# Kernel optimization log

Measured on AMD Instinct MI355X. Metric: run time of the kernel, lower is better.

Reference implementation:

```python
import jax, jax.numpy as jnp
import numpy as np

N_IN = 250000
N_OUT = 500000
INC = 256
OUTC = 128
KVOL = 8  # 2x2x2 transposed-conv kernel volume
BN_EPS = 1e-5


def setup_inputs() -> dict:
    key = jax.random.key(0)
    k1, k2, k3 = jax.random.split(key, 3)
    x = jax.random.normal(k1, (N_IN, INC), dtype=jnp.float32)
    # sparse conv weight: one [inc, outc] matrix per kernel offset
    W = jax.random.normal(k2, (KVOL, INC, OUTC), dtype=jnp.float32) * 0.02
    gamma = jnp.ones((OUTC,), dtype=jnp.float32)
    beta = jnp.zeros((OUTC,), dtype=jnp.float32)
    # kernel map: destination output voxel for each (kernel offset, input voxel)
    out_idx = jax.random.randint(k3, (KVOL, N_IN), 0, N_OUT, dtype=jnp.int32)
    return {"x": x, "W": W, "gamma": gamma, "beta": beta,
            "out_idx": out_idx, "n_out": N_OUT}


def reference(x, W, gamma, beta, out_idx, n_out):
    # --- sparse transposed conv3d: gather-matmul-scatter per kernel offset ---
    out = jnp.zeros((n_out, W.shape[-1]), dtype=x.dtype)
    for k in range(W.shape[0]):  # fixed small kernel volume (8)
        out = out.at[out_idx[k]].add(x @ W[k])
    # --- BatchNorm (training-mode batch stats over all output voxels) ---
    mean = jnp.mean(out, axis=0)
    var = jnp.mean(jnp.square(out - mean), axis=0)
    y = (out - mean) * jax.lax.rsqrt(var + BN_EPS) * gamma + beta
    return y
```

## Files before the change

### kernel.cpp

```cpp
#include <hip/hip_runtime.h>
#include <hip/hip_bf16.h>
#include <stdint.h>

#define N_IN 250000
#define N_OUT 500000
#define INC 256
#define OUTC 128
#define KVOL 8
#define NTOT (KVOL * N_IN)
#define BN_EPS 1e-5f

typedef __bf16 bf16x8_t __attribute__((ext_vector_type(8)));
typedef __bf16 bf16x4_t __attribute__((ext_vector_type(4)));
typedef float f32x4_t __attribute__((ext_vector_type(4)));
typedef uint32_t u32x4_t __attribute__((ext_vector_type(4)));

__device__ __forceinline__ __bf16 f2bf(float x) {
  union { float f; uint32_t u; } v; v.f = x;
  uint32_t r = v.u + 0x7FFFu + ((v.u >> 16) & 1u);
  union { uint16_t s; __bf16 b; } o; o.s = (uint16_t)(r >> 16);
  return o.b;
}

__device__ __forceinline__ uint32_t pack2bf(float lo, float hi) {
  union { float f; uint32_t u; } a, b; a.f = lo; b.f = hi;
  uint32_t ra = a.u + 0x7FFFu + ((a.u >> 16) & 1u);
  uint32_t rb = b.u + 0x7FFFu + ((b.u >> 16) & 1u);
  return (ra >> 16) | (rb & 0xFFFF0000u);
}

__device__ __forceinline__ float bflo(uint32_t w) {
  union { uint32_t u; float f; } v; v.u = w << 16; return v.f;
}
__device__ __forceinline__ float bfhi(uint32_t w) {
  union { uint32_t u; float f; } v; v.u = w & 0xFFFF0000u; return v.f;
}

__global__ void wconv_kernel(const float* __restrict__ W, __bf16* __restrict__ Wt) {
  int f = blockIdx.x * blockDim.x + threadIdx.x;
  if (f >= KVOL * OUTC * INC) return;
  int i = f & (INC - 1);
  int o = (f >> 8) & (OUTC - 1);
  int k = f >> 15;
  Wt[f] = f2bf(W[(k * INC + i) * OUTC + o]);
}


__global__ void hist_kernel(const int* __restrict__ oidx, int* __restrict__ cnt) {
  int g = blockIdx.x * 256 + threadIdx.x;
  if (g < NTOT) atomicAdd(&cnt[oidx[g]], 1);
}

__global__ void scan1_kernel(const int* __restrict__ cnt, int* __restrict__ offs,
                             int* __restrict__ bsum) {
  __shared__ int sd[256];
  int t = threadIdx.x;
  int base = blockIdx.x * 1024 + t * 4;
  int v0 = 0, v1 = 0, v2 = 0, v3 = 0;
  if (base + 3 < N_OUT) {
    int4 v = *(const int4*)&cnt[base];
    v0 = v.x; v1 = v.y; v2 = v.z; v3 = v.w;
  } else {
    if (base     < N_OUT) v0 = cnt[base];
    if (base + 1 < N_OUT) v1 = cnt[base + 1];
    if (base + 2 < N_OUT) v2 = cnt[base + 2];
  }
  int s = v0 + v1 + v2 + v3;
  sd[t] = s; __syncthreads();
  for (int o = 1; o < 256; o <<= 1) {
    int a = (t >= o) ? sd[t - o] : 0;
    __syncthreads();
    sd[t] += a;
    __syncthreads();
  }
  int excl = sd[t] - s;
  if (base     < N_OUT) offs[base]     = excl;
  if (base + 1 < N_OUT) offs[base + 1] = excl + v0;
  if (base + 2 < N_OUT) offs[base + 2] = excl + v0 + v1;
  if (base + 3 < N_OUT) offs[base + 3] = excl + v0 + v1 + v2;
  if (t == 255) bsum[blockIdx.x] = sd[255];
}

__global__ void scan2_kernel(const int* __restrict__ bsum, int* __restrict__ bsumx, int nb) {
  __shared__ int sd[512];
  int t = threadIdx.x;
  int s = (t < nb) ? bsum[t] : 0;
  sd[t] = s; __syncthreads();
  for (int o = 1; o < 512; o <<= 1) {
    int a = (t >= o) ? sd[t - o] : 0;
    __syncthreads();
    sd[t] += a;
    __syncthreads();
  }
  if (t < nb) bsumx[t] = sd[t] - s;
}

__global__ void scan3_kernel(int* __restrict__ offs, int* __restrict__ cursor,
                             const int* __restrict__ bsumx) {
  int g = blockIdx.x * 256 + threadIdx.x;
  if (g < N_OUT) {
    int v = offs[g] + bsumx[g >> 10];
    offs[g] = v;
    cursor[g] = v;
  }
  if (g == 0) offs[N_OUT] = NTOT;
}

__global__ void fill_kernel(const int* __restrict__ oidx, int* __restrict__ cursor,
                            int* __restrict__ slot) {
  int g = blockIdx.x * 256 + threadIdx.x;
  if (g < NTOT) {
    int d = oidx[g];
    slot[g] = atomicAdd(&cursor[d], 1);
  }
}


#define TM 64
#define LDS_STRIDE 264

__global__ __launch_bounds__(512, 1) void gemm_store_kernel(
    const float* __restrict__ x, const __bf16* __restrict__ Wt,
    const int* __restrict__ slot, char* __restrict__ partials) {
  __shared__ __bf16 xs[TM * LDS_STRIDE];
  __shared__ __align__(16) uint2 stg[8][16][34];
  const int t = threadIdx.x;
  const int row0 = blockIdx.x * TM;

  #pragma unroll
  for (int i = 0; i < 8; ++i) {
    int f = t + i * 512;
    int r = f >> 6;
    int c4 = f & 63;
    int grow = row0 + r;
    f32x4_t v = {0.f, 0.f, 0.f, 0.f};
    if (grow < N_IN)
      v = __builtin_nontemporal_load((const f32x4_t*)x + (size_t)grow * 64 + c4);
    bf16x4_t bv;
    bv[0] = f2bf(v[0]); bv[1] = f2bf(v[1]); bv[2] = f2bf(v[2]); bv[3] = f2bf(v[3]);
    *(bf16x4_t*)&xs[r * LDS_STRIDE + c4 * 4] = bv;
  }
  __syncthreads();

  const int w  = t >> 6;
  const int l  = t & 63;
  const int lr = l & 15;
  const int lg = l >> 4;

  f32x4_t accT[8][4];
  #pragma unroll
  for (int n = 0; n < 8; ++n)
    #pragma unroll
    for (int m = 0; m < 4; ++m)
      accT[n][m] = (f32x4_t){0.f, 0.f, 0.f, 0.f};

  const __bf16* Wk = Wt + (size_t)w * OUTC * INC;

  #pragma unroll
  for (int s = 0; s < 8; ++s) {
    bf16x8_t a[4], b[8];
    #pragma unroll
    for (int m = 0; m < 4; ++m)
      a[m] = *(const bf16x8_t*)&xs[(m * 16 + lr) * LDS_STRIDE + s * 32 + lg * 8];
    #pragma unroll
    for (int n = 0; n < 8; ++n)
      b[n] = *(const bf16x8_t*)&Wk[(n * 16 + lr) * INC + s * 32 + lg * 8];
    #pragma unroll
    for (int n = 0; n < 8; ++n)
      #pragma unroll
      for (int m = 0; m < 4; ++m)
        accT[n][m] = __builtin_amdgcn_mfma_f32_16x16x32_bf16(b[n], a[m], accT[n][m], 0, 0, 0);
  }

  const int r2 = l >> 2;
  const int p  = l & 3;
  const int sbase = w * N_IN + row0;
  #pragma unroll
  for (int m = 0; m < 4; ++m) {
    #pragma unroll
    for (int n = 0; n < 8; ++n) {
      uint2 pk;
      pk.x = pack2bf(accT[n][m][0], accT[n][m][1]);
      pk.y = pack2bf(accT[n][m][2], accT[n][m][3]);
      stg[w][lr][n * 4 + lg] = pk;
    }
    asm volatile("s_waitcnt lgkmcnt(0)" ::: "memory");
    __builtin_amdgcn_wave_barrier();
    int grow = row0 + m * 16 + r2;
    if (grow < N_IN) {
      int gs = slot[sbase + m * 16 + r2];
      const u32x4_t* rp = (const u32x4_t*)&stg[w][r2][0];
      char* dst = partials + (size_t)gs * 256 + p * 64;
      #pragma unroll
      for (int q = 0; q < 4; ++q)
        *(u32x4_t*)(dst + q * 16) = rp[p * 4 + q];
    }
    __builtin_amdgcn_wave_barrier();
  }
}


__global__ __launch_bounds__(256) void reduce_stats_kernel(
    const char* __restrict__ partials, const int* __restrict__ offs,
    char* __restrict__ accb, float* __restrict__ stats) {
  const int t = threadIdx.x;
  const int lane16 = t & 15;
  const int grp = t >> 4;
  float s[8], q[8];
  #pragma unroll
  for (int i = 0; i < 8; ++i) { s[i] = 0.f; q[i] = 0.f; }

  for (int d = blockIdx.x * 16 + grp; d < N_OUT; d += gridDim.x * 16) {
    int j0 = offs[d], j1 = offs[d + 1];
    float a[8];
    #pragma unroll
    for (int i = 0; i < 8; ++i) a[i] = 0.f;
    for (int j = j0; j < j1; ++j) {
      u32x4_t v = __builtin_nontemporal_load(
          (const u32x4_t*)(partials + (size_t)j * 256 + lane16 * 16));
      a[0] += bflo(v[0]); a[1] += bfhi(v[0]);
      a[2] += bflo(v[1]); a[3] += bfhi(v[1]);
      a[4] += bflo(v[2]); a[5] += bfhi(v[2]);
      a[6] += bflo(v[3]); a[7] += bfhi(v[3]);
    }
    u32x4_t o;
    o[0] = pack2bf(a[0], a[1]); o[1] = pack2bf(a[2], a[3]);
    o[2] = pack2bf(a[4], a[5]); o[3] = pack2bf(a[6], a[7]);
    *(u32x4_t*)(accb + (size_t)d * 512 + lane16 * 16) = o;
    #pragma unroll
    for (int u = 0; u < 4; ++u) {
      float f0 = bflo(o[u]), f1 = bfhi(o[u]);
      s[2 * u] += f0;     q[2 * u] += f0 * f0;
      s[2 * u + 1] += f1; q[2 * u + 1] += f1 * f1;
    }
  }

  __shared__ float reds[16][16][8];
  __shared__ float redq[16][16][8];
  #pragma unroll
  for (int i = 0; i < 8; ++i) { reds[grp][lane16][i] = s[i]; redq[grp][lane16][i] = q[i]; }
  __syncthreads();
  if (t < 128) {
    float acc = 0.f;
    #pragma unroll
    for (int g2 = 0; g2 < 16; ++g2) acc += reds[g2][t >> 3][t & 7];
    atomicAdd(&stats[t], acc);
  } else {
    int c = t - 128;
    float acc = 0.f;
    #pragma unroll
    for (int g2 = 0; g2 < 16; ++g2) acc += redq[g2][c >> 3][c & 7];
    atomicAdd(&stats[128 + c], acc);
  }
}

__global__ void norm_kernel(char* __restrict__ outb, const float* __restrict__ stats,
                            const float* __restrict__ gamma, const float* __restrict__ beta) {
  const int t = threadIdx.x;
  const int j = t & 15;
  const int ro = t >> 4;
  const float inv_n = 1.0f / (float)N_OUT;
  float sc[8], sh[8];
  #pragma unroll
  for (int i = 0; i < 8; ++i) {
    int c = j * 8 + i;
    float mean = stats[c] * inv_n;
    float var  = stats[128 + c] * inv_n - mean * mean;
    float s = gamma[c] * rsqrtf(var + BN_EPS);
    sc[i] = s;
    sh[i] = beta[c] - mean * s;
  }
  for (int r = blockIdx.x * 16 + ro; r < N_OUT; r += gridDim.x * 16) {
    u32x4_t v = *(const u32x4_t*)(outb + (size_t)r * 512 + j * 16);
    f32x4_t o0, o1;
    #pragma unroll
    for (int u = 0; u < 4; ++u) {
      float f0 = bflo(v[u]) * sc[2 * u] + sh[2 * u];
      float f1 = bfhi(v[u]) * sc[2 * u + 1] + sh[2 * u + 1];
      if (u < 2) { o0[2 * u] = f0; o0[2 * u + 1] = f1; }
      else       { o1[2 * (u - 2)] = f0; o1[2 * (u - 2) + 1] = f1; }
    }
    __builtin_nontemporal_store(o0, (f32x4_t*)(outb + (size_t)r * 512 + j * 32));
    __builtin_nontemporal_store(o1, (f32x4_t*)(outb + (size_t)r * 512 + j * 32 + 16));
  }
}


__global__ __launch_bounds__(512, 1) void gemm_scatter_f32_kernel(
    const float* __restrict__ x, const __bf16* __restrict__ Wt,
    const int* __restrict__ out_idx, float* __restrict__ acc) {
  __shared__ __bf16 xs[TM * LDS_STRIDE];
  const int t = threadIdx.x;
  const int row0 = blockIdx.x * TM;
  #pragma unroll
  for (int i = 0; i < 8; ++i) {
    int f = t + i * 512;
    int r = f >> 6;
    int c4 = f & 63;
    int grow = row0 + r;
    float4 v = make_float4(0.f, 0.f, 0.f, 0.f);
    if (grow < N_IN) v = ((const float4*)x)[(size_t)grow * 64 + c4];
    bf16x4_t bv;
    bv[0] = f2bf(v.x); bv[1] = f2bf(v.y); bv[2] = f2bf(v.z); bv[3] = f2bf(v.w);
    *(bf16x4_t*)&xs[r * LDS_STRIDE + c4 * 4] = bv;
  }
  __syncthreads();
  const int w = t >> 6, l = t & 63, lr = l & 15, lg = l >> 4;
  f32x4_t accr[4][8];
  #pragma unroll
  for (int m = 0; m < 4; ++m)
    #pragma unroll
    for (int n = 0; n < 8; ++n)
      accr[m][n] = (f32x4_t){0.f, 0.f, 0.f, 0.f};
  const __bf16* Wkp = Wt + (size_t)w * OUTC * INC;
  #pragma unroll
  for (int s = 0; s < 8; ++s) {
    bf16x8_t a[4], b[8];
    #pragma unroll
    for (int m = 0; m < 4; ++m)
      a[m] = *(const bf16x8_t*)&xs[(m * 16 + lr) * LDS_STRIDE + s * 32 + lg * 8];
    #pragma unroll
    for (int n = 0; n < 8; ++n)
      b[n] = *(const bf16x8_t*)&Wkp[(n * 16 + lr) * INC + s * 32 + lg * 8];
    #pragma unroll
    for (int m = 0; m < 4; ++m)
      #pragma unroll
      for (int n = 0; n < 8; ++n)
        accr[m][n] = __builtin_amdgcn_mfma_f32_16x16x32_bf16(a[m], b[n], accr[m][n], 0, 0, 0);
  }
  const int* oidx = out_idx + (size_t)w * N_IN;
  #pragma unroll
  for (int m = 0; m < 4; ++m) {
    int rbase = m * 16 + lg * 4;
    #pragma unroll
    for (int reg = 0; reg < 4; ++reg) {
      int grow = row0 + rbase + reg;
      if (grow < N_IN) {
        int dst = oidx[grow];
        float* ap = acc + (size_t)dst * OUTC;
        #pragma unroll
        for (int n = 0; n < 8; ++n)
          atomicAdd(&ap[n * 16 + lr], accr[m][n][reg]);
      }
    }
  }
}

__global__ void stats_f32_kernel(const float* __restrict__ acc, float* __restrict__ stats) {
  const int t = threadIdx.x;
  const int c4 = t & 31;
  const int ro = t >> 5;
  f32x4_t s = {0.f, 0.f, 0.f, 0.f}, q = {0.f, 0.f, 0.f, 0.f};
  for (int r = blockIdx.x * 8 + ro; r < N_OUT; r += gridDim.x * 8) {
    f32x4_t v = ((const f32x4_t*)acc)[(size_t)r * 32 + c4];
    s += v; q += v * v;
  }
  __shared__ float redl[256][8];
  #pragma unroll
  for (int j = 0; j < 4; ++j) { redl[t][j] = s[j]; redl[t][4 + j] = q[j]; }
  __syncthreads();
  if (t < 32) {
    float S[4] = {0.f, 0.f, 0.f, 0.f}, Q[4] = {0.f, 0.f, 0.f, 0.f};
    for (int r2 = 0; r2 < 8; ++r2)
      #pragma unroll
      for (int j = 0; j < 4; ++j) {
        S[j] += redl[r2 * 32 + t][j];
        Q[j] += redl[r2 * 32 + t][4 + j];
      }
    #pragma unroll
    for (int j = 0; j < 4; ++j) {
      atomicAdd(&stats[t * 4 + j], S[j]);
      atomicAdd(&stats[128 + t * 4 + j], Q[j]);
    }
  }
}

__global__ void norm_f32_kernel(float* __restrict__ out, const float* __restrict__ stats,
                                const float* __restrict__ gamma, const float* __restrict__ beta) {
  const int t = threadIdx.x;
  const int c4 = t & 31;
  const int ro = t >> 5;
  const float inv_n = 1.0f / (float)N_OUT;
  float sc[4], sh[4];
  #pragma unroll
  for (int j = 0; j < 4; ++j) {
    int c = c4 * 4 + j;
    float mean = stats[c] * inv_n;
    float var  = stats[128 + c] * inv_n - mean * mean;
    float s = gamma[c] * rsqrtf(var + BN_EPS);
    sc[j] = s;
    sh[j] = beta[c] - mean * s;
  }
  for (int r = blockIdx.x * 8 + ro; r < N_OUT; r += gridDim.x * 8) {
    f32x4_t v = ((const f32x4_t*)out)[(size_t)r * 32 + c4];
    #pragma unroll
    for (int j = 0; j < 4; ++j) v[j] = v[j] * sc[j] + sh[j];
    ((f32x4_t*)out)[(size_t)r * 32 + c4] = v;
  }
}


extern "C" void kernel_launch(void* const* d_in, const int* in_sizes, int n_in,
                              void* d_out, int out_size, void* d_ws, size_t ws_size,
                              hipStream_t stream) {
  const float* x     = (const float*)d_in[0];
  const float* W     = (const float*)d_in[1];
  const float* gamma = (const float*)d_in[2];
  const float* beta  = (const float*)d_in[3];
  const int*   oidx  = (const int*)d_in[4];

  const size_t P_OFF     = 0;
  const size_t SLOT_OFF  = 512000000;
  const size_t CNT_OFF   = 520000000;
  const size_t OFFS_OFF  = 522000000;
  const size_t CURS_OFF  = 524000384;
  const size_t BSUM_OFF  = 526000384;
  const size_t BSUMX_OFF = 526004480;
  const size_t WT_OFF    = 526008576;
  const size_t STATS_OFF = 526532864;
  const size_t NEED      = 526533888;

  if (ws_size >= NEED) {
    char* ws = (char*)d_ws;
    char* partials = ws + P_OFF;
    int* slot   = (int*)(ws + SLOT_OFF);
    int* cnt    = (int*)(ws + CNT_OFF);
    int* offs   = (int*)(ws + OFFS_OFF);
    int* cursor = (int*)(ws + CURS_OFF);
    int* bsum   = (int*)(ws + BSUM_OFF);
    int* bsumx  = (int*)(ws + BSUMX_OFF);
    __bf16* Wt  = (__bf16*)(ws + WT_OFF);
    float* stats = (float*)(ws + STATS_OFF);

    hipMemsetAsync(cnt, 0, N_OUT * sizeof(int), stream);
    hipMemsetAsync(stats, 0, 256 * sizeof(float), stream);

    wconv_kernel<<<(KVOL * OUTC * INC + 255) / 256, 256, 0, stream>>>(W, Wt);
    hist_kernel<<<(NTOT + 255) / 256, 256, 0, stream>>>(oidx, cnt);
    const int NB1 = (N_OUT + 1023) / 1024;
    scan1_kernel<<<NB1, 256, 0, stream>>>(cnt, offs, bsum);
    scan2_kernel<<<1, 512, 0, stream>>>(bsum, bsumx, NB1);
    scan3_kernel<<<(N_OUT + 255) / 256, 256, 0, stream>>>(offs, cursor, bsumx);
    fill_kernel<<<(NTOT + 255) / 256, 256, 0, stream>>>(oidx, cursor, slot);
    gemm_store_kernel<<<(N_IN + TM - 1) / TM, 512, 0, stream>>>(x, Wt, slot, partials);
    reduce_stats_kernel<<<2048, 256, 0, stream>>>(partials, offs, (char*)d_out, stats);
    norm_kernel<<<512, 256, 0, stream>>>((char*)d_out, stats, gamma, beta);
  } else {
    __bf16* Wt   = (__bf16*)d_ws;
    float* stats = (float*)((char*)d_ws + (size_t)KVOL * OUTC * INC * 2);
    float* out = (float*)d_out;

    hipMemsetAsync(d_out, 0, (size_t)N_OUT * OUTC * sizeof(float), stream);
    hipMemsetAsync(stats, 0, 256 * sizeof(float), stream);

    wconv_kernel<<<(KVOL * OUTC * INC + 255) / 256, 256, 0, stream>>>(W, Wt);
    gemm_scatter_f32_kernel<<<(N_IN + TM - 1) / TM, 512, 0, stream>>>(x, Wt, oidx, out);
    stats_f32_kernel<<<1024, 256, 0, stream>>>(out, stats);
    norm_f32_kernel<<<2048, 256, 0, stream>>>(out, stats, gamma, beta);
  }
}
```

Baseline: 855.1 us.

## Replace per-voxel counting sort with coarse 128-voxel buckets and LDS reduction

```diff
diff --git a/kernel.cpp b/kernel.cpp
--- a/kernel.cpp
+++ b/kernel.cpp
@@ -9,6 +9,8 @@
 #define KVOL 8
 #define NTOT (KVOL * N_IN)
 #define BN_EPS 1e-5f
+#define BW_D 128
+#define NB 3907
 
 typedef __bf16 bf16x8_t __attribute__((ext_vector_type(8)));
 typedef __bf16 bf16x4_t __attribute__((ext_vector_type(4)));
@@ -46,82 +48,47 @@
 }
 
 
-__global__ void hist_kernel(const int* __restrict__ oidx, int* __restrict__ cnt) {
+__global__ void histb_kernel(const int* __restrict__ oidx, int* __restrict__ cnt) {
   int g = blockIdx.x * 256 + threadIdx.x;
-  if (g < NTOT) atomicAdd(&cnt[oidx[g]], 1);
-}
-
-__global__ void scan1_kernel(const int* __restrict__ cnt, int* __restrict__ offs,
-                             int* __restrict__ bsum) {
-  __shared__ int sd[256];
-  int t = threadIdx.x;
-  int base = blockIdx.x * 1024 + t * 4;
-  int v0 = 0, v1 = 0, v2 = 0, v3 = 0;
-  if (base + 3 < N_OUT) {
-    int4 v = *(const int4*)&cnt[base];
-    v0 = v.x; v1 = v.y; v2 = v.z; v3 = v.w;
-  } else {
-    if (base     < N_OUT) v0 = cnt[base];
-    if (base + 1 < N_OUT) v1 = cnt[base + 1];
-    if (base + 2 < N_OUT) v2 = cnt[base + 2];
-  }
-  int s = v0 + v1 + v2 + v3;
-  sd[t] = s; __syncthreads();
-  for (int o = 1; o < 256; o <<= 1) {
-    int a = (t >= o) ? sd[t - o] : 0;
-    __syncthreads();
-    sd[t] += a;
-    __syncthreads();
-  }
-  int excl = sd[t] - s;
-  if (base     < N_OUT) offs[base]     = excl;
-  if (base + 1 < N_OUT) offs[base + 1] = excl + v0;
-  if (base + 2 < N_OUT) offs[base + 2] = excl + v0 + v1;
-  if (base + 3 < N_OUT) offs[base + 3] = excl + v0 + v1 + v2;
-  if (t == 255) bsum[blockIdx.x] = sd[255];
-}
-
-__global__ void scan2_kernel(const int* __restrict__ bsum, int* __restrict__ bsumx, int nb) {
+  if (g < NTOT) atomicAdd(&cnt[oidx[g] >> 7], 1);
+}
+
+__global__ void scanb_kernel(const int* __restrict__ cnt, int* __restrict__ base,
+                             int* __restrict__ cur) {
   __shared__ int sd[512];
   int t = threadIdx.x;
-  int s = (t < nb) ? bsum[t] : 0;
-  sd[t] = s; __syncthreads();
+  int v[8]; int sm = 0;
+  #pragma unroll
+  for (int e = 0; e < 8; ++e) {
+    int idx = t * 8 + e;
+    v[e] = (idx < NB) ? cnt[idx] : 0;
+    sm += v[e];
+  }
+  sd[t] = sm; __syncthreads();
   for (int o = 1; o < 512; o <<= 1) {
     int a = (t >= o) ? sd[t - o] : 0;
     __syncthreads();
     sd[t] += a;
     __syncthreads();
   }
-  if (t < nb) bsumx[t] = sd[t] - s;
-}
-
-__global__ void scan3_kernel(int* __restrict__ offs, int* __restrict__ cursor,
-                             const int* __restrict__ bsumx) {
-  int g = blockIdx.x * 256 + threadIdx.x;
-  if (g < N_OUT) {
-    int v = offs[g] + bsumx[g >> 10];
-    offs[g] = v;
-    cursor[g] = v;
-  }
-  if (g == 0) offs[N_OUT] = NTOT;
-}
-
-__global__ void fill_kernel(const int* __restrict__ oidx, int* __restrict__ cursor,
-                            int* __restrict__ slot) {
-  int g = blockIdx.x * 256 + threadIdx.x;
-  if (g < NTOT) {
-    int d = oidx[g];
-    slot[g] = atomicAdd(&cursor[d], 1);
-  }
+  int excl = sd[t] - sm;
+  #pragma unroll
+  for (int e = 0; e < 8; ++e) {
+    int idx = t * 8 + e;
+    if (idx < NB) { base[idx] = excl; cur[idx] = excl; }
+    excl += v[e];
+  }
+  if (t == 511) base[NB] = NTOT;
 }
 
 
 #define TM 64
 #define LDS_STRIDE 264
 
-__global__ __launch_bounds__(512, 1) void gemm_store_kernel(
+__global__ __launch_bounds__(512, 1) void gemm_bin_kernel(
     const float* __restrict__ x, const __bf16* __restrict__ Wt,
-    const int* __restrict__ slot, char* __restrict__ partials) {
+    const int* __restrict__ oidx, int* __restrict__ cur,
+    int* __restrict__ tag, char* __restrict__ partials) {
   __shared__ __bf16 xs[TM * LDS_STRIDE];
   __shared__ __align__(16) uint2 stg[8][16][34];
   const int t = threadIdx.x;
@@ -174,7 +141,6 @@
 
   const int r2 = l >> 2;
   const int p  = l & 3;
-  const int sbase = w * N_IN + row0;
   #pragma unroll
   for (int m = 0; m < 4; ++m) {
     #pragma unroll
@@ -187,10 +153,18 @@
     asm volatile("s_waitcnt lgkmcnt(0)" ::: "memory");
     __builtin_amdgcn_wave_barrier();
     int grow = row0 + m * 16 + r2;
+    int pos = 0;
     if (grow < N_IN) {
-      int gs = slot[sbase + m * 16 + r2];
+      int d = oidx[w * N_IN + grow];
+      if (p == 0) {
+        pos = atomicAdd(&cur[d >> 7], 1);
+        tag[pos] = d;
+      }
+    }
+    pos = __shfl(pos, l & 60, 64);
+    if (grow < N_IN) {
       const u32x4_t* rp = (const u32x4_t*)&stg[w][r2][0];
-      char* dst = partials + (size_t)gs * 256 + p * 64;
+      char* dst = partials + (size_t)pos * 256 + p * 64;
       #pragma unroll
       for (int q = 0; q < 4; ++q)
         *(u32x4_t*)(dst + q * 16) = rp[p * 4 + q];
@@ -200,57 +174,69 @@
 }
 
 
-__global__ __launch_bounds__(256) void reduce_stats_kernel(
-    const char* __restrict__ partials, const int* __restrict__ offs,
-    char* __restrict__ accb, float* __restrict__ stats) {
-  const int t = threadIdx.x;
+__global__ __launch_bounds__(512, 2) void bucket_reduce_kernel(
+    const char* __restrict__ partials, const int* __restrict__ tag,
+    const int* __restrict__ base, char* __restrict__ accb, float* __restrict__ stats) {
+  __shared__ float acc[BW_D][132];
+  __shared__ float reds[4][128];
+  __shared__ float redq[4][128];
+  const int t = threadIdx.x;
+  const int b = blockIdx.x;
+  const int d0 = b * BW_D;
+  const int j0 = base[b], j1 = base[b + 1];
+
+  for (int i = t; i < BW_D * 132; i += 512) ((float*)acc)[i] = 0.f;
+  __syncthreads();
+
   const int lane16 = t & 15;
   const int grp = t >> 4;
-  float s[8], q[8];
-  #pragma unroll
-  for (int i = 0; i < 8; ++i) { s[i] = 0.f; q[i] = 0.f; }
-
-  for (int d = blockIdx.x * 16 + grp; d < N_OUT; d += gridDim.x * 16) {
-    int j0 = offs[d], j1 = offs[d + 1];
-    float a[8];
-    #pragma unroll
-    for (int i = 0; i < 8; ++i) a[i] = 0.f;
-    for (int j = j0; j < j1; ++j) {
-      u32x4_t v = __builtin_nontemporal_load(
-          (const u32x4_t*)(partials + (size_t)j * 256 + lane16 * 16));
-      a[0] += bflo(v[0]); a[1] += bfhi(v[0]);
-      a[2] += bflo(v[1]); a[3] += bfhi(v[1]);
-      a[4] += bflo(v[2]); a[5] += bfhi(v[2]);
-      a[6] += bflo(v[3]); a[7] += bfhi(v[3]);
-    }
-    u32x4_t o;
-    o[0] = pack2bf(a[0], a[1]); o[1] = pack2bf(a[2], a[3]);
-    o[2] = pack2bf(a[4], a[5]); o[3] = pack2bf(a[6], a[7]);
-    *(u32x4_t*)(accb + (size_t)d * 512 + lane16 * 16) = o;
-    #pragma unroll
-    for (int u = 0; u < 4; ++u) {
-      float f0 = bflo(o[u]), f1 = bfhi(o[u]);
-      s[2 * u] += f0;     q[2 * u] += f0 * f0;
-      s[2 * u + 1] += f1; q[2 * u + 1] += f1 * f1;
-    }
-  }
-
-  __shared__ float reds[16][16][8];
-  __shared__ float redq[16][16][8];
-  #pragma unroll
-  for (int i = 0; i < 8; ++i) { reds[grp][lane16][i] = s[i]; redq[grp][lane16][i] = q[i]; }
+  for (int j = j0 + grp; j < j1; j += 32) {
+    int di = tag[j] - d0;
+    u32x4_t v = __builtin_nontemporal_load(
+        (const u32x4_t*)(partials + (size_t)j * 256 + lane16 * 16));
+    float* ap = &acc[di][lane16 * 8];
+    atomicAdd(&ap[0], bflo(v[0])); atomicAdd(&ap[1], bfhi(v[0]));
+    atomicAdd(&ap[2], bflo(v[1])); atomicAdd(&ap[3], bfhi(v[1]));
+    atomicAdd(&ap[4], bflo(v[2])); atomicAdd(&ap[5], bfhi(v[2]));
+    atomicAdd(&ap[6], bflo(v[3])); atomicAdd(&ap[7], bfhi(v[3]));
+  }
+  __syncthreads();
+
+  {
+    int di = t >> 2, q = t & 3;
+    int d = d0 + di;
+    if (d < N_OUT) {
+      uint32_t wbuf[16];
+      #pragma unroll
+      for (int wi = 0; wi < 16; ++wi) {
+        int c = q * 32 + wi * 2;
+        wbuf[wi] = pack2bf(acc[di][c], acc[di][c + 1]);
+      }
+      char* dst = accb + (size_t)d * 512 + q * 64;
+      *(u32x4_t*)dst        = *(u32x4_t*)&wbuf[0];
+      *(u32x4_t*)(dst + 16) = *(u32x4_t*)&wbuf[4];
+      *(u32x4_t*)(dst + 32) = *(u32x4_t*)&wbuf[8];
+      *(u32x4_t*)(dst + 48) = *(u32x4_t*)&wbuf[12];
+    }
+  }
+
+  {
+    int c = t & 127, gr = t >> 7;
+    float sm = 0.f, sq = 0.f;
+    for (int di = gr; di < BW_D; di += 4) {
+      if (d0 + di < N_OUT) {
+        float rv = bflo(pack2bf(acc[di][c], 0.f));
+        sm += rv; sq += rv * rv;
+      }
+    }
+    reds[gr][c] = sm; redq[gr][c] = sq;
+  }
   __syncthreads();
   if (t < 128) {
-    float acc = 0.f;
-    #pragma unroll
-    for (int g2 = 0; g2 < 16; ++g2) acc += reds[g2][t >> 3][t & 7];
-    atomicAdd(&stats[t], acc);
-  } else {
+    atomicAdd(&stats[t], reds[0][t] + reds[1][t] + reds[2][t] + reds[3][t]);
+  } else if (t < 256) {
     int c = t - 128;
-    float acc = 0.f;
-    #pragma unroll
-    for (int g2 = 0; g2 < 16; ++g2) acc += redq[g2][c >> 3][c & 7];
-    atomicAdd(&stats[128 + c], acc);
+    atomicAdd(&stats[128 + c], redq[0][c] + redq[1][c] + redq[2][c] + redq[3][c]);
   }
 }
 
@@ -409,41 +395,35 @@
   const float* beta  = (const float*)d_in[3];
   const int*   oidx  = (const int*)d_in[4];
 
-  const size_t P_OFF     = 0;
-  const size_t SLOT_OFF  = 512000000;
+  const size_t PART_OFF  = 0;
+  const size_t TAG_OFF   = 512000000;
   const size_t CNT_OFF   = 520000000;
-  const size_t OFFS_OFF  = 522000000;
-  const size_t CURS_OFF  = 524000384;
-  const size_t BSUM_OFF  = 526000384;
-  const size_t BSUMX_OFF = 526004480;
-  const size_t WT_OFF    = 526008576;
-  const size_t STATS_OFF = 526532864;
-  const size_t NEED      = 526533888;
+  const size_t BASE_OFF  = 520016384;
+  const size_t CUR_OFF   = 520032768;
+  const size_t WT_OFF    = 520049152;
+  const size_t STATS_OFF = 520573440;
+  const size_t NEED      = 520574464;
 
   if (ws_size >= NEED) {
     char* ws = (char*)d_ws;
-    char* partials = ws + P_OFF;
-    int* slot   = (int*)(ws + SLOT_OFF);
-    int* cnt    = (int*)(ws + CNT_OFF);
-    int* offs   = (int*)(ws + OFFS_OFF);
-    int* cursor = (int*)(ws + CURS_OFF);
-    int* bsum   = (int*)(ws + BSUM_OFF);
-    int* bsumx  = (int*)(ws + BSUMX_OFF);
-    __bf16* Wt  = (__bf16*)(ws + WT_OFF);
+    char* partials = ws + PART_OFF;
+    int* tag     = (int*)(ws + TAG_OFF);
+    int* cnt     = (int*)(ws + CNT_OFF);
+    int* base    = (int*)(ws + BASE_OFF);
+    int* cur     = (int*)(ws + CUR_OFF);
+    __bf16* Wt   = (__bf16*)(ws + WT_OFF);
     float* stats = (float*)(ws + STATS_OFF);
 
-    hipMemsetAsync(cnt, 0, N_OUT * sizeof(int), stream);
+    hipMemsetAsync(cnt, 0, NB * sizeof(int), stream);
     hipMemsetAsync(stats, 0, 256 * sizeof(float), stream);
 
     wconv_kernel<<<(KVOL * OUTC * INC + 255) / 256, 256, 0, stream>>>(W, Wt);
-    hist_kernel<<<(NTOT + 255) / 256, 256, 0, stream>>>(oidx, cnt);
-    const int NB1 = (N_OUT + 1023) / 1024;
-    scan1_kernel<<<NB1, 256, 0, stream>>>(cnt, offs, bsum);
-    scan2_kernel<<<1, 512, 0, stream>>>(bsum, bsumx, NB1);
-    scan3_kernel<<<(N_OUT + 255) / 256, 256, 0, stream>>>(offs, cursor, bsumx);
-    fill_kernel<<<(NTOT + 255) / 256, 256, 0, stream>>>(oidx, cursor, slot);
-    gemm_store_kernel<<<(N_IN + TM - 1) / TM, 512, 0, stream>>>(x, Wt, slot, partials);
-    reduce_stats_kernel<<<2048, 256, 0, stream>>>(partials, offs, (char*)d_out, stats);
+    histb_kernel<<<(NTOT + 255) / 256, 256, 0, stream>>>(oidx, cnt);
+    scanb_kernel<<<1, 512, 0, stream>>>(cnt, base, cur);
+    gemm_bin_kernel<<<(N_IN + TM - 1) / TM, 512, 0, stream>>>(
+        x, Wt, oidx, cur, tag, partials);
+    bucket_reduce_kernel<<<NB, 512, 0, stream>>>(
+        partials, tag, base, (char*)d_out, stats);
     norm_kernel<<<512, 256, 0, stream>>>((char*)d_out, stats, gamma, beta);
   } else {
     __bf16* Wt   = (__bf16*)d_ws;
```

New measurement: 2.103 ms. 146% more time.
